# Performance work log

Measured on AMD Instinct MI355X. Metric: run time of the kernel, lower is better.

The kernel has to match this reference:

```python
import jax, jax.numpy as jnp
import numpy as np

HIDDEN = 2048
NUM_HEADS = 8
NUM_KV_HEADS = 1
HEAD_DIM = 256
ROPE_THETA = 10000.0
T = 2048  # num tokens (single causal prefill sequence)
Q_SIZE = NUM_HEADS * HEAD_DIM        # 2048
KV_SIZE = NUM_KV_HEADS * HEAD_DIM    # 256


def _apply_rope(x, positions):
    # x: [T, n_heads, head_dim], neox style (rotate halves)
    half = HEAD_DIM // 2
    inv_freq = 1.0 / (ROPE_THETA ** (jnp.arange(half, dtype=jnp.float32) * 2.0 / HEAD_DIM))
    ang = positions.astype(jnp.float32)[:, None] * inv_freq[None, :]   # [T, half]
    cos = jnp.cos(ang)[:, None, :]
    sin = jnp.sin(ang)[:, None, :]
    x1, x2 = jnp.split(x, 2, axis=-1)
    return jnp.concatenate([x1 * cos - x2 * sin, x2 * cos + x1 * sin], axis=-1)


def setup_inputs() -> dict:
    key = jax.random.key(0)
    k1, k2, k3 = jax.random.split(key, 3)
    hidden_states = jax.random.normal(k1, (T, HIDDEN), dtype=jnp.float32)
    Wqkv = jax.random.normal(k2, (Q_SIZE + 2 * KV_SIZE, HIDDEN), dtype=jnp.float32) * 0.02
    Wo = jax.random.normal(k3, (HIDDEN, Q_SIZE), dtype=jnp.float32) * 0.02
    positions = jnp.arange(T, dtype=jnp.int32)
    return {"positions": positions, "hidden_states": hidden_states, "Wqkv": Wqkv, "Wo": Wo}


def reference(positions, hidden_states, Wqkv, Wo):
    scaling = HEAD_DIM ** -0.5
    qkv = hidden_states @ Wqkv.T                                   # [T, Q+2KV]
    q = qkv[:, :Q_SIZE].reshape(T, NUM_HEADS, HEAD_DIM)
    k = qkv[:, Q_SIZE:Q_SIZE + KV_SIZE].reshape(T, NUM_KV_HEADS, HEAD_DIM)
    v = qkv[:, Q_SIZE + KV_SIZE:].reshape(T, NUM_KV_HEADS, HEAD_DIM)
    q = _apply_rope(q, positions)
    k = _apply_rope(k, positions)
    # GQA: group query heads over kv heads
    g = NUM_HEADS // NUM_KV_HEADS
    qg = q.reshape(T, NUM_KV_HEADS, g, HEAD_DIM)
    scores = jnp.einsum('qhgd,khd->hgqk', qg, k) * scaling         # [kv, g, T, T]
    causal = jnp.arange(T)[:, None] >= jnp.arange(T)[None, :]
    scores = jnp.where(causal[None, None], scores, jnp.finfo(scores.dtype).min)
    probs = jax.nn.softmax(scores, axis=-1)
    attn = jnp.einsum('hgqk,khd->qhgd', probs, v).reshape(T, Q_SIZE)
    return attn @ Wo.T
```

## Files before the change

### kernel.cpp

```cpp
#include <hip/hip_runtime.h>
#include <hip/hip_bf16.h>

typedef __bf16 bf16x8 __attribute__((ext_vector_type(8)));
typedef __bf16 bf16x4 __attribute__((ext_vector_type(4)));
typedef float floatx4 __attribute__((ext_vector_type(4)));

#define QKV_SLICE 5242880
#define OUT_SLICE 4194304

__device__ __forceinline__ float fast_exp2(float x) {
    return __builtin_amdgcn_exp2f(x);
}

__device__ __forceinline__ void gload16(const __bf16* g, __bf16* l) {
    __builtin_amdgcn_global_load_lds((const __attribute__((address_space(1))) void*)g,
                                     (__attribute__((address_space(3))) void*)l, 16, 0, 0);
}

__global__ __launch_bounds__(256) void cast_all(const float* __restrict__ hid,
                                                const float* __restrict__ wqkv,
                                                const float* __restrict__ wo,
                                                __bf16* __restrict__ Ah,
                                                __bf16* __restrict__ Wqkvh,
                                                __bf16* __restrict__ Woh) {
    const int n1 = 1048576, n2 = 1310720;
    int i = blockIdx.x * 256 + threadIdx.x;
    const float* in;
    __bf16* out;
    int j;
    if (i < n1) { in = hid; out = Ah; j = i; }
    else if (i < n1 + n2) { in = wqkv; out = Wqkvh; j = i - n1; }
    else { in = wo; out = Woh; j = i - n1 - n2; }
    float4 v = ((const float4*)in)[j];
    bf16x4 o;
    o[0] = (__bf16)v.x; o[1] = (__bf16)v.y; o[2] = (__bf16)v.z; o[3] = (__bf16)v.w;
    ((bf16x4*)out)[j] = o;
}

__global__ __launch_bounds__(512) void gemm_bt_256(const __bf16* __restrict__ A,
                                                   const __bf16* __restrict__ B,
                                                   __bf16* __restrict__ C,
                                                   int M, int N, int K) {
    __shared__ __attribute__((aligned(16))) __bf16 As[2][256 * 64];
    __shared__ __attribute__((aligned(16))) __bf16 Bs[2][256 * 64];

    int tid = threadIdx.x, lane = tid & 63, w = tid >> 6;
    int wm = w >> 2, wn = w & 3;
    int bm0 = blockIdx.x * 256, bn0 = blockIdx.y * 256;
    int r = lane & 15, q4 = lane >> 4;
    int Ksl = K / (int)gridDim.z;
    int kbase = (int)blockIdx.z * Ksl;

    int srow = tid >> 3;
    int sslot = (tid & 7) ^ (srow & 7);
    const __bf16* Ag = A + (size_t)(bm0 + srow) * K + kbase + sslot * 8;
    const __bf16* Bg = B + (size_t)(bn0 + srow) * K + kbase + sslot * 8;
    size_t jstep = (size_t)64 * K;
    __bf16* Ald = &As[0][0] + tid * 8;
    __bf16* Bld = &Bs[0][0] + tid * 8;

    floatx4 acc[8][4];
#pragma unroll
    for (int i = 0; i < 8; i++)
#pragma unroll
        for (int j = 0; j < 4; j++) acc[i][j] = (floatx4)0.f;

    int nt = Ksl >> 6;

#pragma unroll
    for (int j = 0; j < 4; j++) {
        gload16(Ag + j * jstep, Ald + j * 4096);
        gload16(Bg + j * jstep, Bld + j * 4096);
    }

    for (int t = 0; t < nt; t++) {
        int cb = t & 1;
        asm volatile("s_waitcnt vmcnt(0)\n\ts_barrier" ::: "memory");
        if (t + 1 < nt) {
            int ko = (t + 1) << 6;
#pragma unroll
            for (int j = 0; j < 4; j++) {
                gload16(Ag + j * jstep + ko, Ald + (cb ^ 1) * 16384 + j * 4096);
                gload16(Bg + j * jstep + ko, Bld + (cb ^ 1) * 16384 + j * 4096);
            }
        }

#pragma unroll
        for (int ks = 0; ks < 2; ks++) {
            bf16x8 a[8], b[4];
#pragma unroll
            for (int m16 = 0; m16 < 8; m16++) {
                int row = wm * 128 + m16 * 16 + r;
                a[m16] = *(const bf16x8*)&As[cb][row * 64 + (((ks << 2) + q4) ^ (r & 7)) * 8];
            }
#pragma unroll
            for (int n16 = 0; n16 < 4; n16++) {
                int row = wn * 64 + n16 * 16 + r;
                b[n16] = *(const bf16x8*)&Bs[cb][row * 64 + (((ks << 2) + q4) ^ (r & 7)) * 8];
            }
            __builtin_amdgcn_s_setprio(1);
#pragma unroll
            for (int m16 = 0; m16 < 8; m16++)
#pragma unroll
                for (int n16 = 0; n16 < 4; n16++)
                    acc[m16][n16] = __builtin_amdgcn_mfma_f32_16x16x32_bf16(a[m16], b[n16], acc[m16][n16], 0, 0, 0);
            __builtin_amdgcn_s_setprio(0);
        }
    }

    __bf16* Cp = C + (size_t)blockIdx.z * M * N;
#pragma unroll
    for (int m16 = 0; m16 < 8; m16++)
#pragma unroll
        for (int n16 = 0; n16 < 4; n16++) {
            int row = bm0 + wm * 128 + m16 * 16 + q4 * 4;
            int col = bn0 + wn * 64 + n16 * 16 + r;
#pragma unroll
            for (int i = 0; i < 4; i++)
                Cp[(size_t)(row + i) * N + col] = (__bf16)acc[m16][n16][i];
        }
}

__global__ __launch_bounds__(256) void rope_vtrans(const __bf16* __restrict__ qp,
                                                   const int* __restrict__ positions,
                                                   __bf16* __restrict__ Qo,
                                                   __bf16* __restrict__ Ko,
                                                   __bf16* __restrict__ Vt) {
    __shared__ float tile[32][33];
    int b = blockIdx.x;
    if (b < 9216) {
        int idx = b * 256 + threadIdx.x;
        int i = idx & 127;
        int th = idx >> 7;
        int head = th % 9;
        int t = th / 9;
        float invf = expf(-(float)i * 0.07195578415606394f);
        float ang = (float)positions[t] * invf;
        float s = sinf(ang), c = cosf(ang);
        size_t off = (size_t)t * 2560 + (head < 8 ? head * 256 : 2048);
        float x1 = 0.f, x2 = 0.f;
#pragma unroll
        for (int sp = 0; sp < 4; sp++) {
            x1 += (float)qp[sp * QKV_SLICE + off + i];
            x2 += (float)qp[sp * QKV_SLICE + off + i + 128];
        }
        if (head < 8) {
            const float qs = 0.09016844f;
            __bf16* dst = Qo + (size_t)t * 2048 + head * 256;
            dst[i]       = (__bf16)((x1 * c - x2 * s) * qs);
            dst[i + 128] = (__bf16)((x2 * c + x1 * s) * qs);
        } else {
            int sw = (t & 7) << 3;
            __bf16* dst = Ko + (size_t)t * 256;
            dst[i ^ sw]         = (__bf16)(x1 * c - x2 * s);
            dst[(i + 128) ^ sw] = (__bf16)(x2 * c + x1 * s);
        }
    } else {
        int bb = b - 9216;
        int bt = bb & 63;
        int bc = bb >> 6;
        int tx = threadIdx.x & 31;
        int ty0 = threadIdx.x >> 5;
#pragma unroll
        for (int ty = ty0; ty < 32; ty += 8) {
            size_t gi = (size_t)(bt * 32 + ty) * 2560 + 2304 + bc * 32 + tx;
            float v = 0.f;
#pragma unroll
            for (int sp = 0; sp < 4; sp++) v += (float)qp[sp * QKV_SLICE + gi];
            tile[ty][tx] = v;
        }
        __syncthreads();
#pragma unroll
        for (int ty = ty0; ty < 32; ty += 8)
            Vt[(size_t)bt * 8192 + (bc * 2 + (ty >> 4)) * 512 + (ty & 15) * 8
               + (tx >> 3) * 128 + (tx & 7)] = (__bf16)tile[tx][ty];
    }
}

__global__ __launch_bounds__(256, 2) void attn_kernel(const __bf16* __restrict__ Q,
                                                      const __bf16* __restrict__ Kg,
                                                      const __bf16* __restrict__ Vt,
                                                      __bf16* __restrict__ Opart,
                                                      float2* __restrict__ Ml) {
    __shared__ __attribute__((aligned(16))) __bf16 Ks[2][32 * 256];
    __shared__ __attribute__((aligned(16))) __bf16 Vs[2][16 * 512];
    __shared__ __attribute__((aligned(16))) __bf16 Ps[4][32][40];

    int hg = blockIdx.x;
    int rs = 203 - (int)blockIdx.y;
    int k, base;
    if (rs < 12)       { k = 1; base = 0; }
    else if (rs < 36)  { k = 2; base = 12; }
    else if (rs < 72)  { k = 3; base = 36; }
    else if (rs < 120) { k = 4; base = 72; }
    else if (rs < 180) { k = 5; base = 120; }
    else               { k = 6; base = 180; }
    int idx = rs - base;
    int s = idx % k;
    int g = (k - 1) * 12 + idx / k;
    int slot = base + idx - s;

    int start = s * 384;
    int end = g * 32 + 32;
    if (end > start + 384) end = start + 384;
    int ntiles = (end - start) >> 5;

    int tid = threadIdx.x, lane = tid & 63, w = tid >> 6;
    int r = lane & 15, q4 = lane >> 4;
    int h = hg * 4 + w;
    int sw = (r & 7) << 3;

    bf16x8 qf[2][8];
#pragma unroll
    for (int qt = 0; qt < 2; qt++) {
        const __bf16* qrow = Q + (size_t)(g * 32 + qt * 16 + r) * 2048 + h * 256 + q4 * 8;
#pragma unroll
        for (int ks = 0; ks < 8; ks++) qf[qt][ks] = *(const bf16x8*)(qrow + ks * 32);
    }

    bf16x8 ones;
#pragma unroll
    for (int i = 0; i < 8; i++) ones[i] = (__bf16)1.0f;

    floatx4 acc[2][16];
#pragma unroll
    for (int qt = 0; qt < 2; qt++)
#pragma unroll
        for (int i = 0; i < 16; i++) acc[qt][i] = (floatx4)0.f;
    floatx4 acc_l[2];
    acc_l[0] = (floatx4)0.f; acc_l[1] = (floatx4)0.f;

    {
        const __bf16* kp = Kg + (size_t)start * 256 + tid * 8;
        const __bf16* vp = Vt + (size_t)(start >> 5) * 8192 + tid * 8;
        __bf16* kl = &Ks[0][tid * 8];
        __bf16* vl = &Vs[0][tid * 8];
#pragma unroll
        for (int j = 0; j < 4; j++) {
            gload16(kp + j * 2048, kl + j * 2048);
            gload16(vp + j * 2048, vl + j * 2048);
        }
    }

    for (int t = 0; t < ntiles; t++) {
        int cb = t & 1;
        int kt0 = start + t * 32;
        asm volatile("s_barrier" ::: "memory");
        if (t + 1 < ntiles) {
            int kt1 = kt0 + 32;
            const __bf16* kp = Kg + (size_t)kt1 * 256 + tid * 8;
            const __bf16* vp = Vt + (size_t)(kt1 >> 5) * 8192 + tid * 8;
            __bf16* kl = &Ks[cb ^ 1][tid * 8];
            __bf16* vl = &Vs[cb ^ 1][tid * 8];
#pragma unroll
            for (int j = 0; j < 4; j++) {
                gload16(kp + j * 2048, kl + j * 2048);
                gload16(vp + j * 2048, vl + j * 2048);
            }
            asm volatile("s_waitcnt vmcnt(8)\n\ts_barrier" ::: "memory");
        } else {
            asm volatile("s_waitcnt vmcnt(0)\n\ts_barrier" ::: "memory");
        }

        floatx4 sc[2][2];
        sc[0][0] = (floatx4)0.f; sc[0][1] = (floatx4)0.f;
        sc[1][0] = (floatx4)0.f; sc[1][1] = (floatx4)0.f;
#pragma unroll
        for (int ks = 0; ks < 8; ks++) {
#pragma unroll
            for (int nt = 0; nt < 2; nt++) {
                bf16x8 kf = *(const bf16x8*)&Ks[cb][(nt * 16 + r) * 256 + ((ks * 32 + q4 * 8) ^ sw)];
#pragma unroll
                for (int qt = 0; qt < 2; qt++)
                    sc[qt][nt] = __builtin_amdgcn_mfma_f32_16x16x32_bf16(qf[qt][ks], kf, sc[qt][nt], 0, 0, 0);
            }
        }
        if (kt0 + 31 > g * 32) {
#pragma unroll
            for (int qt = 0; qt < 2; qt++) {
                int qbase = g * 32 + qt * 16 + q4 * 4;
#pragma unroll
                for (int nt = 0; nt < 2; nt++) {
                    int kpos = kt0 + nt * 16 + r;
#pragma unroll
                    for (int i = 0; i < 4; i++)
                        if (kpos > qbase + i) sc[qt][nt][i] = -3e38f;
                }
            }
        }

#pragma unroll
        for (int qt = 0; qt < 2; qt++)
#pragma unroll
            for (int nt = 0; nt < 2; nt++)
#pragma unroll
                for (int i = 0; i < 4; i++)
                    Ps[w][qt * 16 + q4 * 4 + i][(nt * 16 + r) ^ (q4 << 3)] = (__bf16)fast_exp2(sc[qt][nt][i]);
        __builtin_amdgcn_wave_barrier();
        bf16x8 pf[2];
#pragma unroll
        for (int qt = 0; qt < 2; qt++)
            pf[qt] = *(const bf16x8*)&Ps[w][qt * 16 + r][(q4 * 8) ^ ((r >> 2) << 3)];
        __builtin_amdgcn_wave_barrier();

#pragma unroll
        for (int n16 = 0; n16 < 16; n16++) {
            bf16x8 vf = *(const bf16x8*)&Vs[cb][n16 * 512 + lane * 8];
            acc[0][n16] = __builtin_amdgcn_mfma_f32_16x16x32_bf16(pf[0], vf, acc[0][n16], 0, 0, 0);
            acc[1][n16] = __builtin_amdgcn_mfma_f32_16x16x32_bf16(pf[1], vf, acc[1][n16], 0, 0, 0);
        }
        acc_l[0] = __builtin_amdgcn_mfma_f32_16x16x32_bf16(pf[0], ones, acc_l[0], 0, 0, 0);
        acc_l[1] = __builtin_amdgcn_mfma_f32_16x16x32_bf16(pf[1], ones, acc_l[1], 0, 0, 0);
    }

    size_t base_row = (size_t)(slot + s) * 256 + hg * 128 + w * 32;
#pragma unroll
    for (int qt = 0; qt < 2; qt++)
#pragma unroll
        for (int n16 = 0; n16 < 16; n16++)
#pragma unroll
            for (int i = 0; i < 4; i++)
                Opart[(base_row + qt * 16 + q4 * 4 + i) * 256 + n16 * 16 + r] = (__bf16)acc[qt][n16][i];
    if (r == 0) {
#pragma unroll
        for (int qt = 0; qt < 2; qt++)
#pragma unroll
            for (int i = 0; i < 4; i++)
                Ml[base_row + qt * 16 + q4 * 4 + i] = make_float2(0.f, acc_l[qt][i]);
    }
}

__global__ __launch_bounds__(256) void combine_kernel(const __bf16* __restrict__ Opart,
                                                      const float2* __restrict__ Ml,
                                                      __bf16* __restrict__ attnb) {
    int wid = blockIdx.x * 4 + (threadIdx.x >> 6);
    int lane = threadIdx.x & 63;
    int t = wid >> 3, h = wid & 7;
    int g = t >> 5, r32 = t & 31;
    int qt = r32 >> 4, row16 = r32 & 15;
    int hg = h >> 2, w = h & 3;
    int k = g / 12 + 1;
    int fg = 6 * k * (k - 1) + (g - 12 * (k - 1)) * k;

    float ls[6];
    size_t rbase[6];
    for (int s = 0; s < k; s++) {
        rbase[s] = (size_t)(fg + s) * 256 + hg * 128 + w * 32 + qt * 16 + row16;
        ls[s] = Ml[rbase[s]].y;
    }
    float L = 0.f;
    float o[4] = {0.f, 0.f, 0.f, 0.f};
    for (int s = 0; s < k; s++) {
        L += ls[s];
        bf16x4 v = *(const bf16x4*)&Opart[rbase[s] * 256 + lane * 4];
#pragma unroll
        for (int j = 0; j < 4; j++) o[j] += (float)v[j];
    }
    float inv = 1.f / L;
    bf16x4 ov;
#pragma unroll
    for (int j = 0; j < 4; j++) ov[j] = (__bf16)(o[j] * inv);
    *(bf16x4*)&attnb[(size_t)t * 2048 + h * 256 + lane * 4] = ov;
}

__global__ __launch_bounds__(256) void add_out(const __bf16* __restrict__ p,
                                               float* __restrict__ out, int n4) {
    int i = blockIdx.x * 256 + threadIdx.x;
    if (i < n4) {
        float o[4] = {0.f, 0.f, 0.f, 0.f};
#pragma unroll
        for (int s = 0; s < 4; s++) {
            bf16x4 a = ((const bf16x4*)(p + (size_t)s * OUT_SLICE))[i];
#pragma unroll
            for (int j = 0; j < 4; j++) o[j] += (float)a[j];
        }
        float4 ov;
        ov.x = o[0]; ov.y = o[1]; ov.z = o[2]; ov.w = o[3];
        ((float4*)out)[i] = ov;
    }
}

extern "C" void kernel_launch(void* const* d_in, const int* in_sizes, int n_in,
                              void* d_out, int out_size, void* d_ws, size_t ws_size,
                              hipStream_t stream) {
    const int* positions = (const int*)d_in[0];
    const float* hidden  = (const float*)d_in[1];
    const float* Wqkv    = (const float*)d_in[2];
    const float* Wo      = (const float*)d_in[3];
    float* out = (float*)d_out;

    char* ws = (char*)d_ws;
    const size_t MB = 1024 * 1024;
    __bf16* Ah    = (__bf16*)(ws + 0 * MB);
    __bf16* Woh   = (__bf16*)(ws + 8 * MB);
    __bf16* Qb    = (__bf16*)(ws + 16 * MB);
    __bf16* Kb    = (__bf16*)(ws + 24 * MB);
    __bf16* Vtb   = (__bf16*)(ws + 25 * MB);
    __bf16* Wqkvh = (__bf16*)(ws + 26 * MB);
    __bf16* qkvp  = (__bf16*)(ws + 36 * MB);
    __bf16* Opart = (__bf16*)(ws + 26 * MB);
    float2* Ml    = (float2*)(ws + 52 * MB);
    __bf16* attnb = Ah;
    __bf16* gp    = (__bf16*)(ws + 26 * MB);

    cast_all<<<13312, 256, 0, stream>>>(hidden, Wqkv, Wo, Ah, Wqkvh, Woh);

    gemm_bt_256<<<dim3(8, 10, 4), 512, 0, stream>>>(Ah, Wqkvh, qkvp, 2048, 2560, 2048);

    rope_vtrans<<<9728, 256, 0, stream>>>(qkvp, positions, Qb, Kb, Vtb);

    attn_kernel<<<dim3(2, 204), 256, 0, stream>>>(Qb, Kb, Vtb, Opart, Ml);
    combine_kernel<<<4096, 256, 0, stream>>>(Opart, Ml, attnb);

    gemm_bt_256<<<dim3(8, 8, 4), 512, 0, stream>>>(attnb, Woh, gp, 2048, 2048, 2048);
    add_out<<<4096, 256, 0, stream>>>(gp, out, 1048576);
}
```

Measured before the change: 229.9 us.

## Interleave GEMM global prefetch with LDS reads and MFMA phases

Restructures the GEMM main loop into four phases per K-tile. Each phase loads half of the A fragments (and B on alternate phases) from LDS, issues one slice of the next tile's global-to-LDS loads, then runs 16 MFMAs between barriers. The goal is to spread memory traffic across the compute so that prefetch and LDS latency overlap with MFMA, in a ping-pong style. The cost is more barriers per tile, and correctness depends on the barrier ordering around the double buffer.

```diff
diff --git a/kernel.cpp b/kernel.cpp
--- a/kernel.cpp
+++ b/kernel.cpp
@@ -68,43 +68,52 @@
     int nt = Ksl >> 6;
 
 #pragma unroll
-    for (int j = 0; j < 4; j++) {
-        gload16(Ag + j * jstep, Ald + j * 4096);
-        gload16(Bg + j * jstep, Bld + j * 4096);
-    }
+    for (int p = 0; p < 4; p++) {
+        gload16(Ag + p * jstep, Ald + p * 4096);
+        gload16(Bg + p * jstep, Bld + p * 4096);
+    }
+    asm volatile("s_waitcnt vmcnt(0)" ::: "memory");
+    __builtin_amdgcn_s_barrier();
 
     for (int t = 0; t < nt; t++) {
         int cb = t & 1;
-        asm volatile("s_waitcnt vmcnt(0)\n\ts_barrier" ::: "memory");
+        bf16x8 b[4];
+#pragma unroll
+        for (int p = 0; p < 4; p++) {
+            int ks = p >> 1, mh = p & 1;
+            bf16x8 a[4];
+#pragma unroll
+            for (int f = 0; f < 4; f++) {
+                int row = wm * 128 + mh * 64 + f * 16 + r;
+                a[f] = *(const bf16x8*)&As[cb][row * 64 + (((ks << 2) + q4) ^ (r & 7)) * 8];
+            }
+            if (mh == 0) {
+#pragma unroll
+                for (int n16 = 0; n16 < 4; n16++) {
+                    int row = wn * 64 + n16 * 16 + r;
+                    b[n16] = *(const bf16x8*)&Bs[cb][row * 64 + (((ks << 2) + q4) ^ (r & 7)) * 8];
+                }
+            }
+            if (t + 1 < nt) {
+                int ko = (t + 1) << 6;
+                gload16(Ag + p * jstep + ko, Ald + (cb ^ 1) * 16384 + p * 4096);
+                gload16(Bg + p * jstep + ko, Bld + (cb ^ 1) * 16384 + p * 4096);
+            }
+            __builtin_amdgcn_s_barrier();
+            asm volatile("s_waitcnt lgkmcnt(0)" ::: "memory");
+            __builtin_amdgcn_s_setprio(1);
+#pragma unroll
+            for (int f = 0; f < 4; f++)
+#pragma unroll
+                for (int n16 = 0; n16 < 4; n16++)
+                    acc[mh * 4 + f][n16] =
+                        __builtin_amdgcn_mfma_f32_16x16x32_bf16(a[f], b[n16], acc[mh * 4 + f][n16], 0, 0, 0);
+            __builtin_amdgcn_s_setprio(0);
+            __builtin_amdgcn_s_barrier();
+        }
         if (t + 1 < nt) {
-            int ko = (t + 1) << 6;
-#pragma unroll
-            for (int j = 0; j < 4; j++) {
-                gload16(Ag + j * jstep + ko, Ald + (cb ^ 1) * 16384 + j * 4096);
-                gload16(Bg + j * jstep + ko, Bld + (cb ^ 1) * 16384 + j * 4096);
-            }
-        }
-
-#pragma unroll
-        for (int ks = 0; ks < 2; ks++) {
-            bf16x8 a[8], b[4];
-#pragma unroll
-            for (int m16 = 0; m16 < 8; m16++) {
-                int row = wm * 128 + m16 * 16 + r;
-                a[m16] = *(const bf16x8*)&As[cb][row * 64 + (((ks << 2) + q4) ^ (r & 7)) * 8];
-            }
-#pragma unroll
-            for (int n16 = 0; n16 < 4; n16++) {
-                int row = wn * 64 + n16 * 16 + r;
-                b[n16] = *(const bf16x8*)&Bs[cb][row * 64 + (((ks << 2) + q4) ^ (r & 7)) * 8];
-            }
-            __builtin_amdgcn_s_setprio(1);
-#pragma unroll
-            for (int m16 = 0; m16 < 8; m16++)
-#pragma unroll
-                for (int n16 = 0; n16 < 4; n16++)
-                    acc[m16][n16] = __builtin_amdgcn_mfma_f32_16x16x32_bf16(a[m16], b[n16], acc[m16][n16], 0, 0, 0);
-            __builtin_amdgcn_s_setprio(0);
+            asm volatile("s_waitcnt vmcnt(0)" ::: "memory");
+            __builtin_amdgcn_s_barrier();
         }
     }
 
```

New measurement: 226.5 us. Within noise of the previous version (-1.5%).
